# Optimization experiments

Hardware: AMD Instinct MI355X
Metric: run time of the kernel (lower is better)

The kernel has to match this reference:

```python
import jax, jax.numpy as jnp
import numpy as np

IN_SIZE = 1024
HID = 1024


def setup_inputs() -> dict:
    key = jax.random.key(0)
    ks = jax.random.split(key, 8)
    B = 8192
    comb = IN_SIZE + 2 * HID
    scale = 1.0 / np.sqrt(comb)
    inp = {
        "x": jax.random.normal(ks[0], (B, IN_SIZE), jnp.float32),
        "h_left": jax.random.normal(ks[1], (B, HID), jnp.float32),
        "c_left": jax.random.normal(ks[2], (B, HID), jnp.float32),
        "h_right": jax.random.normal(ks[3], (B, HID), jnp.float32),
        "c_right": jax.random.normal(ks[4], (B, HID), jnp.float32),
        # Stacked weights for the 5 gates: [i, f_left, f_right, o, u]
        "W": jax.random.uniform(ks[5], (5 * HID, comb), jnp.float32, -scale, scale),
        "b": jax.random.uniform(ks[6], (5 * HID,), jnp.float32, -scale, scale),
    }
    return inp


def reference(x, h_left, c_left, h_right, c_right, W, b):
    # combined: (B, input_size + 2*hidden_size)
    combined = jnp.concatenate([x, h_left, h_right], axis=1)
    # One fused GEMM for all 5 gates: (B, 5H)
    gates = combined @ W.T + b
    i, fl, fr, o, u = jnp.split(gates, 5, axis=1)
    i = jax.nn.sigmoid(i)
    fl = jax.nn.sigmoid(fl)
    fr = jax.nn.sigmoid(fr)
    o = jax.nn.sigmoid(o)
    u = jnp.tanh(u)
    c = i * u + fl * c_left + fr * c_right
    h = o * jnp.tanh(c)
    return (h, c)
```

## Files before the change

### kernel.cpp

```cpp
#include <hip/hip_runtime.h>
#include <stdint.h>

typedef unsigned int u32;
typedef short short8 __attribute__((ext_vector_type(8)));
typedef short bf16x8 __attribute__((ext_vector_type(8)));
typedef float f32x4  __attribute__((ext_vector_type(4)));

#define B_ROWS 8192
#define HID    1024
#define KDIM   3072
#define NGATE  5

#define BM 256
#define BN 320
#define BK 64
#define NT (KDIM / BK)
#define LDSA_SH (BM * BK)
#define LDSB_SH (BN * BK)
#define BUF_SH  (LDSA_SH + LDSB_SH)
#define BUF_BYTES (BUF_SH * 2)

__device__ __forceinline__ short f2bf(float f) {
  u32 u = __builtin_bit_cast(u32, f);
  u += 0x7FFFu + ((u >> 16) & 1u);
  return (short)(u >> 16);
}

__device__ __forceinline__ float sigf(float v) { return 1.0f / (1.0f + __expf(-v)); }

__device__ __forceinline__ void async_copy16(const void* g, void* l) {
  __builtin_amdgcn_global_load_lds(
      (__attribute__((address_space(1))) void*)(g),
      (__attribute__((address_space(3))) void*)(l),
      16, 0, 0);
}

__global__ void convert_combined(const float* __restrict__ x,
                                 const float* __restrict__ hl,
                                 const float* __restrict__ hr,
                                 short* __restrict__ out) {
  const int total  = B_ROWS * (KDIM / 8);
  const int stride = gridDim.x * blockDim.x;
  for (int i = blockIdx.x * blockDim.x + threadIdx.x; i < total; i += stride) {
    int row = i / (KDIM / 8);
    int col = (i - row * (KDIM / 8)) * 8;
    const float* src;
    if (col < 1024)      src = x  + (int64_t)row * 1024 + col;
    else if (col < 2048) src = hl + (int64_t)row * 1024 + (col - 1024);
    else                 src = hr + (int64_t)row * 1024 + (col - 2048);
    float4 v0 = ((const float4*)src)[0];
    float4 v1 = ((const float4*)src)[1];
    short8 r;
    r[0] = f2bf(v0.x); r[1] = f2bf(v0.y); r[2] = f2bf(v0.z); r[3] = f2bf(v0.w);
    r[4] = f2bf(v1.x); r[5] = f2bf(v1.y); r[6] = f2bf(v1.z); r[7] = f2bf(v1.w);
    *(short8*)(out + (int64_t)row * KDIM + col) = r;
  }
}

__global__ void convert_w(const float* __restrict__ Wf, short* __restrict__ out) {
  const int total  = NGATE * HID * (KDIM / 8);
  const int stride = gridDim.x * blockDim.x;
  for (int i = blockIdx.x * blockDim.x + threadIdx.x; i < total; i += stride) {
    int64_t e = (int64_t)i * 8;
    float4 v0 = ((const float4*)(Wf + e))[0];
    float4 v1 = ((const float4*)(Wf + e))[1];
    short8 r;
    r[0] = f2bf(v0.x); r[1] = f2bf(v0.y); r[2] = f2bf(v0.z); r[3] = f2bf(v0.w);
    r[4] = f2bf(v1.x); r[5] = f2bf(v1.y); r[6] = f2bf(v1.z); r[7] = f2bf(v1.w);
    *(short8*)(out + e) = r;
  }
}

__global__ __launch_bounds__(512, 2) void lstm_gemm(
    const short* __restrict__ Abf,
    const short* __restrict__ Wbf,
    const float* __restrict__ bias,
    const float* __restrict__ c_left,
    const float* __restrict__ c_right,
    float* __restrict__ out) {
  __shared__ short lds[2 * BUF_SH];
  char* const ldsc = (char*)lds;

  const int tid = threadIdx.x;
  const int w  = tid >> 6;
  const int l  = tid & 63;
  const int wm = w >> 2;
  const int wn = w & 3;
  const int lc = l & 15;
  const int khalf = l >> 4;

  const int bid = blockIdx.x;
  const int wg  = (bid & 7) * 64 + (bid >> 3);
  const int m0  = (wg >> 4) * BM;
  const int j0  = (wg & 15) * 64;

  const int r8 = l >> 3;
  const int sl = (l & 7) ^ r8;
  u32 aoff[4], boff[5];
#pragma unroll
  for (int i = 0; i < 4; ++i)
    aoff[i] = (u32)(m0 + (w * 4 + i) * 8 + r8) * KDIM + sl * 8;
#pragma unroll
  for (int i = 0; i < 5; ++i) {
    int rb = (w * 5 + i) * 8 + r8;
    int g  = (rb % 80) >> 4;
    int dj = (rb / 80) * 16 + (rb & 15);
    boff[i] = (u32)(g * HID + j0 + dj) * KDIM + sl * 8;
  }

  const u32 sw0 = (u32)(((khalf    ) ^ (lc & 7)) * 16);
  const u32 sw1 = (u32)(((khalf + 4) ^ (lc & 7)) * 16);
  u32 aAd0 = (u32)((wm * 128 + lc) * 128) + sw0;
  u32 aAd1 = (u32)((wm * 128 + lc) * 128) + sw1;
  u32 bAd0 = (u32)(LDSA_SH * 2) + (u32)((wn * 80 + lc) * 128) + sw0;
  u32 bAd1 = (u32)(LDSA_SH * 2) + (u32)((wn * 80 + lc) * 128) + sw1;

  f32x4 acc[8][5];
  const f32x4 zero = {0.0f, 0.0f, 0.0f, 0.0f};
#pragma unroll
  for (int m = 0; m < 8; ++m)
#pragma unroll
    for (int n = 0; n < 5; ++n) acc[m][n] = zero;

#pragma unroll
  for (int i = 0; i < 4; ++i)
    async_copy16(Abf + aoff[i], lds + (w * 4 + i) * 512);
#pragma unroll
  for (int i = 0; i < 5; ++i)
    async_copy16(Wbf + boff[i], lds + LDSA_SH + (w * 5 + i) * 512);
#pragma unroll
  for (int i = 0; i < 4; ++i) aoff[i] += BK;
#pragma unroll
  for (int i = 0; i < 5; ++i) boff[i] += BK;
  asm volatile("s_waitcnt vmcnt(0)" ::: "memory");
  __builtin_amdgcn_s_barrier();

  int bufd = BUF_BYTES;
  for (int t = 0; t < NT; ++t) {
    if (t < NT - 1) {
      short* dA = lds + ((t + 1) & 1) * BUF_SH;
      short* dB = dA + LDSA_SH;
#pragma unroll
      for (int i = 0; i < 4; ++i)
        async_copy16(Abf + aoff[i], dA + (w * 4 + i) * 512);
#pragma unroll
      for (int i = 0; i < 5; ++i)
        async_copy16(Wbf + boff[i], dB + (w * 5 + i) * 512);
#pragma unroll
      for (int i = 0; i < 4; ++i) aoff[i] += BK;
#pragma unroll
      for (int i = 0; i < 5; ++i) boff[i] += BK;
    }

    bf16x8 bfr[5][2];
#pragma unroll
    for (int nf = 0; nf < 5; ++nf) {
      bfr[nf][0] = *(const bf16x8*)(ldsc + bAd0 + nf * 2048);
      bfr[nf][1] = *(const bf16x8*)(ldsc + bAd1 + nf * 2048);
    }

#pragma unroll
    for (int p = 0; p < 4; ++p) {
      bf16x8 af[2][2];
#pragma unroll
      for (int mf = 0; mf < 2; ++mf) {
        af[mf][0] = *(const bf16x8*)(ldsc + aAd0 + (p * 32 + mf * 16) * 128);
        af[mf][1] = *(const bf16x8*)(ldsc + aAd1 + (p * 32 + mf * 16) * 128);
      }
      __builtin_amdgcn_s_setprio(1);
#pragma unroll
      for (int mf = 0; mf < 2; ++mf)
#pragma unroll
        for (int nf = 0; nf < 5; ++nf)
#pragma unroll
          for (int kk = 0; kk < 2; ++kk)
            acc[p * 2 + mf][nf] = __builtin_amdgcn_mfma_f32_16x16x32_bf16(
                af[mf][kk], bfr[nf][kk], acc[p * 2 + mf][nf], 0, 0, 0);
      __builtin_amdgcn_s_setprio(0);
    }

    asm volatile("s_waitcnt vmcnt(0) lgkmcnt(0)" ::: "memory");
    __builtin_amdgcn_s_barrier();

    aAd0 += bufd; aAd1 += bufd; bAd0 += bufd; bAd1 += bufd;
    bufd = -bufd;
  }

  const int j = j0 + wn * 16 + lc;
  float bi[5];
#pragma unroll
  for (int g = 0; g < 5; ++g) bi[g] = bias[g * HID + j];
#pragma unroll
  for (int m = 0; m < 8; ++m) {
#pragma unroll
    for (int r = 0; r < 4; ++r) {
      const int row = m0 + wm * 128 + m * 16 + khalf * 4 + r;
      const int off = row * HID + j;
      float iv  = sigf(acc[m][0][r] + bi[0]);
      float flv = sigf(acc[m][1][r] + bi[1]);
      float frv = sigf(acc[m][2][r] + bi[2]);
      float ov  = sigf(acc[m][3][r] + bi[3]);
      float uv  = tanhf(acc[m][4][r] + bi[4]);
      float cv  = iv * uv + flv * c_left[off] + frv * c_right[off];
      out[off] = ov * tanhf(cv);
      out[B_ROWS * HID + off] = cv;
    }
  }
}

__global__ void lstm_fallback(const float* __restrict__ x, const float* __restrict__ hl,
                              const float* __restrict__ hr, const float* __restrict__ cl,
                              const float* __restrict__ cr, const float* __restrict__ W,
                              const float* __restrict__ b, float* __restrict__ out) {
  int64_t idx = (int64_t)blockIdx.x * blockDim.x + threadIdx.x;
  if (idx >= (int64_t)B_ROWS * HID) return;
  int bi = (int)(idx >> 10);
  int j  = (int)(idx & 1023);
  float acc[5];
#pragma unroll
  for (int g = 0; g < 5; ++g) acc[g] = b[g * HID + j];
  const float* segs[3] = {x + (int64_t)bi * 1024, hl + (int64_t)bi * 1024,
                          hr + (int64_t)bi * 1024};
  for (int s = 0; s < 3; ++s) {
    const float4* v = (const float4*)segs[s];
    for (int k4 = 0; k4 < 256; ++k4) {
      float4 a = v[k4];
#pragma unroll
      for (int g = 0; g < 5; ++g) {
        const float4 wv = *(const float4*)(W + (int64_t)(g * HID + j) * KDIM + s * 1024 + k4 * 4);
        acc[g] += a.x * wv.x + a.y * wv.y + a.z * wv.z + a.w * wv.w;
      }
    }
  }
  float iv = sigf(acc[0]), fl = sigf(acc[1]), fr = sigf(acc[2]), ov = sigf(acc[3]);
  float uv = tanhf(acc[4]);
  float cv = iv * uv + fl * cl[idx] + fr * cr[idx];
  out[idx] = ov * tanhf(cv);
  out[(int64_t)B_ROWS * HID + idx] = cv;
}

extern "C" void kernel_launch(void* const* d_in, const int* in_sizes, int n_in,
                              void* d_out, int out_size, void* d_ws, size_t ws_size,
                              hipStream_t stream) {
  const float* x  = (const float*)d_in[0];
  const float* hl = (const float*)d_in[1];
  const float* cl = (const float*)d_in[2];
  const float* hr = (const float*)d_in[3];
  const float* cr = (const float*)d_in[4];
  const float* W  = (const float*)d_in[5];
  const float* b  = (const float*)d_in[6];
  float* out = (float*)d_out;

  const size_t needA = (size_t)B_ROWS * KDIM * sizeof(short);
  const size_t needW = (size_t)NGATE * HID * KDIM * sizeof(short);

  if (ws_size >= needA + needW) {
    short* Abf = (short*)d_ws;
    short* Wbf = (short*)((char*)d_ws + needA);
    convert_combined<<<2048, 256, 0, stream>>>(x, hl, hr, Abf);
    convert_w<<<2048, 256, 0, stream>>>(W, Wbf);
    lstm_gemm<<<512, 512, 0, stream>>>(Abf, Wbf, b, cl, cr, out);
  } else {
    lstm_fallback<<<(B_ROWS * HID) / 256, 256, 0, stream>>>(x, hl, hr, cl, cr, W, b, out);
  }
}
```

Baseline: 291.5 us.

## Make GEMM persistent over two M-tiles with deeper, finer-grained load pipeline

Each workgroup now processes two M tiles (256 blocks instead of 512), so the K loop runs twice and the epilogue for the first tile runs mid-kernel. Global-to-LDS loads are issued two stages ahead, spread across waves and sub-phases of the MFMA loop, with partial vmcnt waits and per-phase barriers replacing the full drain at each K step. The intent is to hide load latency and make the grid a single wave on the device. In exchange there are many more barriers per K step, more complex wait counts, and a possible hazard from writing buffer (T+2)&1, which is the same LDS buffer being read at step T.

```diff
diff --git a/kernel.cpp b/kernel.cpp
--- a/kernel.cpp
+++ b/kernel.cpp
@@ -15,6 +15,7 @@
 #define BN 320
 #define BK 64
 #define NT (KDIM / BK)
+#define NTT (2 * NT)
 #define LDSA_SH (BM * BK)
 #define LDSB_SH (BN * BK)
 #define BUF_SH  (LDSA_SH + LDSB_SH)
@@ -86,27 +87,46 @@
   const int l  = tid & 63;
   const int wm = w >> 2;
   const int wn = w & 3;
+  const int wsel = w & 3;
   const int lc = l & 15;
   const int khalf = l >> 4;
 
   const int bid = blockIdx.x;
-  const int wg  = (bid & 7) * 64 + (bid >> 3);
-  const int m0  = (wg >> 4) * BM;
-  const int j0  = (wg & 15) * 64;
+  const int wg  = (bid & 7) * 32 + (bid >> 3);
+  const int mb  = wg >> 4;
+  const int jb  = wg & 15;
+  const int j0  = jb * 64;
+  const u32 aBase0 = (u32)(mb * BM) * KDIM;
+  const u32 aBase1 = aBase0 + (u32)(16 * BM) * KDIM;
 
   const int r8 = l >> 3;
   const int sl = (l & 7) ^ r8;
-  u32 aoff[4], boff[5];
+  u32 laneA[4], laneB[5];
 #pragma unroll
   for (int i = 0; i < 4; ++i)
-    aoff[i] = (u32)(m0 + (w * 4 + i) * 8 + r8) * KDIM + sl * 8;
+    laneA[i] = (u32)((w * 4 + i) * 8 + r8) * KDIM + sl * 8;
 #pragma unroll
   for (int i = 0; i < 5; ++i) {
     int rb = (w * 5 + i) * 8 + r8;
     int g  = (rb % 80) >> 4;
     int dj = (rb / 80) * 16 + (rb & 15);
-    boff[i] = (u32)(g * HID + j0 + dj) * KDIM + sl * 8;
-  }
+    laneB[i] = (u32)(g * HID + j0 + dj) * KDIM + sl * 8;
+  }
+
+  auto stageA = [&](int s) {
+    const u32 off = (s >= NT ? aBase1 + (u32)(s - NT) * BK : aBase0 + (u32)s * BK);
+    short* dst = lds + (s & 1) * BUF_SH + w * 2048;
+#pragma unroll
+    for (int i = 0; i < 4; ++i)
+      async_copy16(Abf + laneA[i] + off, dst + i * 512);
+  };
+  auto stageB = [&](int s) {
+    const u32 off = (u32)(s >= NT ? s - NT : s) * BK;
+    short* dst = lds + (s & 1) * BUF_SH + LDSA_SH + w * 2560;
+#pragma unroll
+    for (int i = 0; i < 5; ++i)
+      async_copy16(Wbf + laneB[i] + off, dst + i * 512);
+  };
 
   const u32 sw0 = (u32)(((khalf    ) ^ (lc & 7)) * 16);
   const u32 sw1 = (u32)(((khalf + 4) ^ (lc & 7)) * 16);
@@ -122,51 +142,65 @@
 #pragma unroll
     for (int n = 0; n < 5; ++n) acc[m][n] = zero;
 
-#pragma unroll
-  for (int i = 0; i < 4; ++i)
-    async_copy16(Abf + aoff[i], lds + (w * 4 + i) * 512);
-#pragma unroll
-  for (int i = 0; i < 5; ++i)
-    async_copy16(Wbf + boff[i], lds + LDSA_SH + (w * 5 + i) * 512);
-#pragma unroll
-  for (int i = 0; i < 4; ++i) aoff[i] += BK;
-#pragma unroll
-  for (int i = 0; i < 5; ++i) boff[i] += BK;
-  asm volatile("s_waitcnt vmcnt(0)" ::: "memory");
+  const int j = j0 + wn * 16 + lc;
+  auto epilogue = [&](int m0) {
+    float bi[5];
+#pragma unroll
+    for (int g = 0; g < 5; ++g) bi[g] = bias[g * HID + j];
+#pragma unroll
+    for (int m = 0; m < 8; ++m) {
+#pragma unroll
+      for (int r = 0; r < 4; ++r) {
+        const int row = m0 + wm * 128 + m * 16 + khalf * 4 + r;
+        const int off = row * HID + j;
+        float iv  = sigf(acc[m][0][r] + bi[0]);
+        float flv = sigf(acc[m][1][r] + bi[1]);
+        float frv = sigf(acc[m][2][r] + bi[2]);
+        float ov  = sigf(acc[m][3][r] + bi[3]);
+        float uv  = tanhf(acc[m][4][r] + bi[4]);
+        float cv  = iv * uv + flv * c_left[off] + frv * c_right[off];
+        out[off] = ov * tanhf(cv);
+        out[B_ROWS * HID + off] = cv;
+      }
+    }
+  };
+
+  stageA(0); stageB(0);
+  stageA(1); stageB(1);
+  asm volatile("s_waitcnt vmcnt(9)" ::: "memory");
   __builtin_amdgcn_s_barrier();
 
   int bufd = BUF_BYTES;
-  for (int t = 0; t < NT; ++t) {
-    if (t < NT - 1) {
-      short* dA = lds + ((t + 1) & 1) * BUF_SH;
-      short* dB = dA + LDSA_SH;
-#pragma unroll
-      for (int i = 0; i < 4; ++i)
-        async_copy16(Abf + aoff[i], dA + (w * 4 + i) * 512);
-#pragma unroll
-      for (int i = 0; i < 5; ++i)
-        async_copy16(Wbf + boff[i], dB + (w * 5 + i) * 512);
-#pragma unroll
-      for (int i = 0; i < 4; ++i) aoff[i] += BK;
-#pragma unroll
-      for (int i = 0; i < 5; ++i) boff[i] += BK;
-    }
-
+  for (int T = 0; T < NTT; ++T) {
     bf16x8 bfr[5][2];
 #pragma unroll
-    for (int nf = 0; nf < 5; ++nf) {
-      bfr[nf][0] = *(const bf16x8*)(ldsc + bAd0 + nf * 2048);
-      bfr[nf][1] = *(const bf16x8*)(ldsc + bAd1 + nf * 2048);
-    }
-
-#pragma unroll
     for (int p = 0; p < 4; ++p) {
+      if (p == 0) {
+#pragma unroll
+        for (int nf = 0; nf < 5; ++nf) {
+          bfr[nf][0] = *(const bf16x8*)(ldsc + bAd0 + nf * 2048);
+          bfr[nf][1] = *(const bf16x8*)(ldsc + bAd1 + nf * 2048);
+        }
+      }
       bf16x8 af[2][2];
 #pragma unroll
       for (int mf = 0; mf < 2; ++mf) {
         af[mf][0] = *(const bf16x8*)(ldsc + aAd0 + (p * 32 + mf * 16) * 128);
         af[mf][1] = *(const bf16x8*)(ldsc + aAd1 + (p * 32 + mf * 16) * 128);
       }
+      if (p == 0) {
+        if (wsel == 3 && T >= 1 && T + 1 < NTT) stageA(T + 1);
+      } else if (p == 1) {
+        if (T + 2 < NTT) { stageB(T + 2); if (wsel == 0) stageA(T + 2); }
+      } else if (p == 2) {
+        if (wsel == 1 && T + 2 < NTT) stageA(T + 2);
+      } else {
+        if (wsel == 2 && T + 2 < NTT) stageA(T + 2);
+      }
+      __builtin_amdgcn_sched_barrier(0);
+      __builtin_amdgcn_s_barrier();
+      asm volatile("s_waitcnt lgkmcnt(0)" ::: "memory");
+      __builtin_amdgcn_sched_barrier(0);
       __builtin_amdgcn_s_setprio(1);
 #pragma unroll
       for (int mf = 0; mf < 2; ++mf)
@@ -177,35 +211,29 @@
             acc[p * 2 + mf][nf] = __builtin_amdgcn_mfma_f32_16x16x32_bf16(
                 af[mf][kk], bfr[nf][kk], acc[p * 2 + mf][nf], 0, 0, 0);
       __builtin_amdgcn_s_setprio(0);
-    }
-
-    asm volatile("s_waitcnt vmcnt(0) lgkmcnt(0)" ::: "memory");
-    __builtin_amdgcn_s_barrier();
-
+      __builtin_amdgcn_sched_barrier(0);
+      if (p == 3) {
+        if (T < NTT - 2) {
+          if (wsel == 3) asm volatile("s_waitcnt vmcnt(5)" ::: "memory");
+          else           asm volatile("s_waitcnt vmcnt(9)" ::: "memory");
+        } else if (T == NTT - 2) {
+          asm volatile("s_waitcnt vmcnt(0)" ::: "memory");
+        }
+      }
+      __builtin_amdgcn_s_barrier();
+    }
     aAd0 += bufd; aAd1 += bufd; bAd0 += bufd; bAd1 += bufd;
     bufd = -bufd;
-  }
-
-  const int j = j0 + wn * 16 + lc;
-  float bi[5];
-#pragma unroll
-  for (int g = 0; g < 5; ++g) bi[g] = bias[g * HID + j];
-#pragma unroll
-  for (int m = 0; m < 8; ++m) {
-#pragma unroll
-    for (int r = 0; r < 4; ++r) {
-      const int row = m0 + wm * 128 + m * 16 + khalf * 4 + r;
-      const int off = row * HID + j;
-      float iv  = sigf(acc[m][0][r] + bi[0]);
-      float flv = sigf(acc[m][1][r] + bi[1]);
-      float frv = sigf(acc[m][2][r] + bi[2]);
-      float ov  = sigf(acc[m][3][r] + bi[3]);
-      float uv  = tanhf(acc[m][4][r] + bi[4]);
-      float cv  = iv * uv + flv * c_left[off] + frv * c_right[off];
-      out[off] = ov * tanhf(cv);
-      out[B_ROWS * HID + off] = cv;
-    }
-  }
+
+    if (T == NT - 1) {
+      epilogue(mb * BM);
+#pragma unroll
+      for (int m = 0; m < 8; ++m)
+#pragma unroll
+        for (int n = 0; n < 5; ++n) acc[m][n] = zero;
+    }
+  }
+  epilogue(mb * BM + 16 * BM);
 }
 
 __global__ void lstm_fallback(const float* __restrict__ x, const float* __restrict__ hl,
@@ -259,7 +287,7 @@
     short* Wbf = (short*)((char*)d_ws + needA);
     convert_combined<<<2048, 256, 0, stream>>>(x, hl, hr, Abf);
     convert_w<<<2048, 256, 0, stream>>>(W, Wbf);
-    lstm_gemm<<<512, 512, 0, stream>>>(Abf, Wbf, b, cl, cr, out);
+    lstm_gemm<<<256, 512, 0, stream>>>(Abf, Wbf, b, cl, cr, out);
   } else {
     lstm_fallback<<<(B_ROWS * HID) / 256, 256, 0, stream>>>(x, hl, hr, cl, cr, W, b, out);
   }
```

Result: slower. 467.4 us (+60.4%).

## Prefetch two K-tiles ahead with staggered per-wave staging and partial vmcnt waits

Applied to the files above, without the earlier changes.

Restructures the LDS double-buffer pipeline so global loads run two K-steps ahead. A-tile staging is spread across the four p-phases by wave index, and waits use partial vmcnt counts instead of draining to zero. This aims to hide global memory latency behind the MFMA work. It adds two barriers per p-phase (eight per K-step), and the buffer reuse with only two LDS buffers relies on the per-phase barriers for correctness.

```diff
diff --git a/kernel.cpp b/kernel.cpp
--- a/kernel.cpp
+++ b/kernel.cpp
@@ -86,6 +86,7 @@
   const int l  = tid & 63;
   const int wm = w >> 2;
   const int wn = w & 3;
+  const int wsel = w & 3;
   const int lc = l & 15;
   const int khalf = l >> 4;
 
@@ -107,6 +108,29 @@
     int dj = (rb / 80) * 16 + (rb & 15);
     boff[i] = (u32)(g * HID + j0 + dj) * KDIM + sl * 8;
   }
+  u32 stA = 0, stB = 0;
+
+#define STAGE_A()                                                          \
+  do {                                                                     \
+    short* dA_ = (short*)(ldsc + stA);                                     \
+    _Pragma("unroll")                                                      \
+    for (int i_ = 0; i_ < 4; ++i_)                                         \
+      async_copy16(Abf + aoff[i_], dA_ + (w * 4 + i_) * 512);              \
+    _Pragma("unroll")                                                      \
+    for (int i_ = 0; i_ < 4; ++i_) aoff[i_] += BK;                         \
+    stA ^= BUF_BYTES;                                                      \
+  } while (0)
+
+#define STAGE_B()                                                          \
+  do {                                                                     \
+    short* dB_ = (short*)(ldsc + stB) + LDSA_SH;                           \
+    _Pragma("unroll")                                                      \
+    for (int i_ = 0; i_ < 5; ++i_)                                         \
+      async_copy16(Wbf + boff[i_], dB_ + (w * 5 + i_) * 512);              \
+    _Pragma("unroll")                                                      \
+    for (int i_ = 0; i_ < 5; ++i_) boff[i_] += BK;                         \
+    stB ^= BUF_BYTES;                                                      \
+  } while (0)
 
   const u32 sw0 = (u32)(((khalf    ) ^ (lc & 7)) * 16);
   const u32 sw1 = (u32)(((khalf + 4) ^ (lc & 7)) * 16);
@@ -122,51 +146,42 @@
 #pragma unroll
     for (int n = 0; n < 5; ++n) acc[m][n] = zero;
 
-#pragma unroll
-  for (int i = 0; i < 4; ++i)
-    async_copy16(Abf + aoff[i], lds + (w * 4 + i) * 512);
-#pragma unroll
-  for (int i = 0; i < 5; ++i)
-    async_copy16(Wbf + boff[i], lds + LDSA_SH + (w * 5 + i) * 512);
-#pragma unroll
-  for (int i = 0; i < 4; ++i) aoff[i] += BK;
-#pragma unroll
-  for (int i = 0; i < 5; ++i) boff[i] += BK;
-  asm volatile("s_waitcnt vmcnt(0)" ::: "memory");
+  STAGE_A(); STAGE_B();
+  STAGE_A(); STAGE_B();
+  asm volatile("s_waitcnt vmcnt(9)" ::: "memory");
   __builtin_amdgcn_s_barrier();
 
   int bufd = BUF_BYTES;
   for (int t = 0; t < NT; ++t) {
-    if (t < NT - 1) {
-      short* dA = lds + ((t + 1) & 1) * BUF_SH;
-      short* dB = dA + LDSA_SH;
-#pragma unroll
-      for (int i = 0; i < 4; ++i)
-        async_copy16(Abf + aoff[i], dA + (w * 4 + i) * 512);
-#pragma unroll
-      for (int i = 0; i < 5; ++i)
-        async_copy16(Wbf + boff[i], dB + (w * 5 + i) * 512);
-#pragma unroll
-      for (int i = 0; i < 4; ++i) aoff[i] += BK;
-#pragma unroll
-      for (int i = 0; i < 5; ++i) boff[i] += BK;
-    }
-
+    const bool canP = (t <= NT - 3);
     bf16x8 bfr[5][2];
 #pragma unroll
-    for (int nf = 0; nf < 5; ++nf) {
-      bfr[nf][0] = *(const bf16x8*)(ldsc + bAd0 + nf * 2048);
-      bfr[nf][1] = *(const bf16x8*)(ldsc + bAd1 + nf * 2048);
-    }
-
-#pragma unroll
     for (int p = 0; p < 4; ++p) {
+      if (p == 0) {
+#pragma unroll
+        for (int nf = 0; nf < 5; ++nf) {
+          bfr[nf][0] = *(const bf16x8*)(ldsc + bAd0 + nf * 2048);
+          bfr[nf][1] = *(const bf16x8*)(ldsc + bAd1 + nf * 2048);
+        }
+      }
       bf16x8 af[2][2];
 #pragma unroll
       for (int mf = 0; mf < 2; ++mf) {
         af[mf][0] = *(const bf16x8*)(ldsc + aAd0 + (p * 32 + mf * 16) * 128);
         af[mf][1] = *(const bf16x8*)(ldsc + aAd1 + (p * 32 + mf * 16) * 128);
       }
+      if (p == 0) {
+        if (wsel == 3 && t >= 1 && t <= NT - 2) STAGE_A();
+      } else if (p == 1) {
+        if (canP) STAGE_B();
+        if (wsel == 0 && canP) STAGE_A();
+      } else if (p == 2) {
+        if (wsel == 1 && canP) STAGE_A();
+      } else {
+        if (wsel == 2 && canP) STAGE_A();
+      }
+      __builtin_amdgcn_s_barrier();
+      asm volatile("s_waitcnt lgkmcnt(0)" ::: "memory");
       __builtin_amdgcn_s_setprio(1);
 #pragma unroll
       for (int mf = 0; mf < 2; ++mf)
@@ -177,11 +192,16 @@
             acc[p * 2 + mf][nf] = __builtin_amdgcn_mfma_f32_16x16x32_bf16(
                 af[mf][kk], bfr[nf][kk], acc[p * 2 + mf][nf], 0, 0, 0);
       __builtin_amdgcn_s_setprio(0);
+      if (p == 3) {
+        if (t < NT - 2) {
+          if (wsel == 3) asm volatile("s_waitcnt vmcnt(5)" ::: "memory");
+          else           asm volatile("s_waitcnt vmcnt(9)" ::: "memory");
+        } else if (t == NT - 2) {
+          asm volatile("s_waitcnt vmcnt(0)" ::: "memory");
+        }
+      }
+      __builtin_amdgcn_s_barrier();
     }
-
-    asm volatile("s_waitcnt vmcnt(0) lgkmcnt(0)" ::: "memory");
-    __builtin_amdgcn_s_barrier();
-
     aAd0 += bufd; aAd1 += bufd; bAd0 += bufd; bAd1 += bufd;
     bufd = -bufd;
   }
```

New measurement: 323.7 us. 1.11x slower.

## Double GEMM block to 16 waves with smaller per-wave 64x80 tiles

Applied to the files above, without the earlier changes.

Raises the GEMM block from 512 to 1024 threads. Each wave now computes a 64x80 output tile instead of 128x80, and the global-to-LDS copies are spread over 16 waves. The MFMA inner loop is reordered to run one k-half at a time, loading B fragments once and streaming one A fragment per row block, with the priority raise now covering the whole tile. The aim is more resident waves per CU to hide LDS and global latency, at the cost of less register-level reuse per wave and more LDS reads per MFMA.

```diff
diff --git a/kernel.cpp b/kernel.cpp
--- a/kernel.cpp
+++ b/kernel.cpp
@@ -71,7 +71,7 @@
   }
 }
 
-__global__ __launch_bounds__(512, 2) void lstm_gemm(
+__global__ __launch_bounds__(1024, 4) void lstm_gemm(
     const short* __restrict__ Abf,
     const short* __restrict__ Wbf,
     const float* __restrict__ bias,
@@ -96,42 +96,48 @@
 
   const int r8 = l >> 3;
   const int sl = (l & 7) ^ r8;
-  u32 aoff[4], boff[5];
-#pragma unroll
-  for (int i = 0; i < 4; ++i)
-    aoff[i] = (u32)(m0 + (w * 4 + i) * 8 + r8) * KDIM + sl * 8;
-#pragma unroll
-  for (int i = 0; i < 5; ++i) {
-    int rb = (w * 5 + i) * 8 + r8;
-    int g  = (rb % 80) >> 4;
-    int dj = (rb / 80) * 16 + (rb & 15);
-    boff[i] = (u32)(g * HID + j0 + dj) * KDIM + sl * 8;
+  u32 aoff[2];
+#pragma unroll
+  for (int i = 0; i < 2; ++i)
+    aoff[i] = (u32)(m0 + (2 * w + i) * 8 + r8) * KDIM + sl * 8;
+  u32 boff[3];
+#pragma unroll
+  for (int i = 0; i < 3; ++i) {
+    int lb = w + 16 * i;
+    if (lb < 40) {
+      int rb = lb * 8 + r8;
+      int g  = (rb % 80) >> 4;
+      int dj = (rb / 80) * 16 + (rb & 15);
+      boff[i] = (u32)(g * HID + j0 + dj) * KDIM + sl * 8;
+    } else boff[i] = boff[0];
   }
 
   const u32 sw0 = (u32)(((khalf    ) ^ (lc & 7)) * 16);
   const u32 sw1 = (u32)(((khalf + 4) ^ (lc & 7)) * 16);
-  u32 aAd0 = (u32)((wm * 128 + lc) * 128) + sw0;
-  u32 aAd1 = (u32)((wm * 128 + lc) * 128) + sw1;
+  u32 aAd0 = (u32)((wm * 64 + lc) * 128) + sw0;
+  u32 aAd1 = (u32)((wm * 64 + lc) * 128) + sw1;
   u32 bAd0 = (u32)(LDSA_SH * 2) + (u32)((wn * 80 + lc) * 128) + sw0;
   u32 bAd1 = (u32)(LDSA_SH * 2) + (u32)((wn * 80 + lc) * 128) + sw1;
 
-  f32x4 acc[8][5];
+  f32x4 acc[4][5];
   const f32x4 zero = {0.0f, 0.0f, 0.0f, 0.0f};
 #pragma unroll
-  for (int m = 0; m < 8; ++m)
+  for (int m = 0; m < 4; ++m)
 #pragma unroll
     for (int n = 0; n < 5; ++n) acc[m][n] = zero;
 
 #pragma unroll
-  for (int i = 0; i < 4; ++i)
-    async_copy16(Abf + aoff[i], lds + (w * 4 + i) * 512);
-#pragma unroll
-  for (int i = 0; i < 5; ++i)
-    async_copy16(Wbf + boff[i], lds + LDSA_SH + (w * 5 + i) * 512);
-#pragma unroll
-  for (int i = 0; i < 4; ++i) aoff[i] += BK;
-#pragma unroll
-  for (int i = 0; i < 5; ++i) boff[i] += BK;
+  for (int i = 0; i < 2; ++i)
+    async_copy16(Abf + aoff[i], lds + (2 * w + i) * 512);
+#pragma unroll
+  for (int i = 0; i < 2; ++i)
+    async_copy16(Wbf + boff[i], lds + LDSA_SH + (w + 16 * i) * 512);
+  if (w < 8)
+    async_copy16(Wbf + boff[2], lds + LDSA_SH + (32 + w) * 512);
+#pragma unroll
+  for (int i = 0; i < 2; ++i) aoff[i] += BK;
+#pragma unroll
+  for (int i = 0; i < 3; ++i) boff[i] += BK;
   asm volatile("s_waitcnt vmcnt(0)" ::: "memory");
   __builtin_amdgcn_s_barrier();
 
@@ -141,43 +147,49 @@
       short* dA = lds + ((t + 1) & 1) * BUF_SH;
       short* dB = dA + LDSA_SH;
 #pragma unroll
-      for (int i = 0; i < 4; ++i)
-        async_copy16(Abf + aoff[i], dA + (w * 4 + i) * 512);
-#pragma unroll
-      for (int i = 0; i < 5; ++i)
-        async_copy16(Wbf + boff[i], dB + (w * 5 + i) * 512);
-#pragma unroll
-      for (int i = 0; i < 4; ++i) aoff[i] += BK;
-#pragma unroll
-      for (int i = 0; i < 5; ++i) boff[i] += BK;
-    }
-
-    bf16x8 bfr[5][2];
-#pragma unroll
-    for (int nf = 0; nf < 5; ++nf) {
-      bfr[nf][0] = *(const bf16x8*)(ldsc + bAd0 + nf * 2048);
-      bfr[nf][1] = *(const bf16x8*)(ldsc + bAd1 + nf * 2048);
-    }
-
-#pragma unroll
-    for (int p = 0; p < 4; ++p) {
-      bf16x8 af[2][2];
-#pragma unroll
-      for (int mf = 0; mf < 2; ++mf) {
-        af[mf][0] = *(const bf16x8*)(ldsc + aAd0 + (p * 32 + mf * 16) * 128);
-        af[mf][1] = *(const bf16x8*)(ldsc + aAd1 + (p * 32 + mf * 16) * 128);
+      for (int i = 0; i < 2; ++i)
+        async_copy16(Abf + aoff[i], dA + (2 * w + i) * 512);
+#pragma unroll
+      for (int i = 0; i < 2; ++i)
+        async_copy16(Wbf + boff[i], dB + (w + 16 * i) * 512);
+      if (w < 8)
+        async_copy16(Wbf + boff[2], dB + (32 + w) * 512);
+#pragma unroll
+      for (int i = 0; i < 2; ++i) aoff[i] += BK;
+#pragma unroll
+      for (int i = 0; i < 3; ++i) boff[i] += BK;
+    }
+
+    __builtin_amdgcn_s_setprio(1);
+    {
+      bf16x8 bfr[5];
+#pragma unroll
+      for (int g = 0; g < 5; ++g)
+        bfr[g] = *(const bf16x8*)(ldsc + bAd0 + g * 2048);
+#pragma unroll
+      for (int m = 0; m < 4; ++m) {
+        bf16x8 af = *(const bf16x8*)(ldsc + aAd0 + m * 2048);
+#pragma unroll
+        for (int g = 0; g < 5; ++g)
+          acc[m][g] = __builtin_amdgcn_mfma_f32_16x16x32_bf16(
+              af, bfr[g], acc[m][g], 0, 0, 0);
       }
-      __builtin_amdgcn_s_setprio(1);
-#pragma unroll
-      for (int mf = 0; mf < 2; ++mf)
-#pragma unroll
-        for (int nf = 0; nf < 5; ++nf)
-#pragma unroll
-          for (int kk = 0; kk < 2; ++kk)
-            acc[p * 2 + mf][nf] = __builtin_amdgcn_mfma_f32_16x16x32_bf16(
-                af[mf][kk], bfr[nf][kk], acc[p * 2 + mf][nf], 0, 0, 0);
-      __builtin_amdgcn_s_setprio(0);
-    }
+    }
+    {
+      bf16x8 bfr[5];
+#pragma unroll
+      for (int g = 0; g < 5; ++g)
+        bfr[g] = *(const bf16x8*)(ldsc + bAd1 + g * 2048);
+#pragma unroll
+      for (int m = 0; m < 4; ++m) {
+        bf16x8 af = *(const bf16x8*)(ldsc + aAd1 + m * 2048);
+#pragma unroll
+        for (int g = 0; g < 5; ++g)
+          acc[m][g] = __builtin_amdgcn_mfma_f32_16x16x32_bf16(
+              af, bfr[g], acc[m][g], 0, 0, 0);
+      }
+    }
+    __builtin_amdgcn_s_setprio(0);
 
     asm volatile("s_waitcnt vmcnt(0) lgkmcnt(0)" ::: "memory");
     __builtin_amdgcn_s_barrier();
@@ -191,10 +203,10 @@
 #pragma unroll
   for (int g = 0; g < 5; ++g) bi[g] = bias[g * HID + j];
 #pragma unroll
-  for (int m = 0; m < 8; ++m) {
+  for (int m = 0; m < 4; ++m) {
 #pragma unroll
     for (int r = 0; r < 4; ++r) {
-      const int row = m0 + wm * 128 + m * 16 + khalf * 4 + r;
+      const int row = m0 + wm * 64 + m * 16 + khalf * 4 + r;
       const int off = row * HID + j;
       float iv  = sigf(acc[m][0][r] + bi[0]);
       float flv = sigf(acc[m][1][r] + bi[1]);
@@ -259,7 +271,7 @@
     short* Wbf = (short*)((char*)d_ws + needA);
     convert_combined<<<2048, 256, 0, stream>>>(x, hl, hr, Abf);
     convert_w<<<2048, 256, 0, stream>>>(W, Wbf);
-    lstm_gemm<<<512, 512, 0, stream>>>(Abf, Wbf, b, cl, cr, out);
+    lstm_gemm<<<512, 1024, 0, stream>>>(Abf, Wbf, b, cl, cr, out);
   } else {
     lstm_fallback<<<(B_ROWS * HID) / 256, 256, 0, stream>>>(x, hl, hr, cl, cr, W, b, out);
   }
```

New measurement: 274.2 us. -5.9%, faster.
